# Performance work log

Hardware: AMD Instinct MI355X
Metric: run time of the kernel (lower is better)

Reference implementation:

```python
import jax, jax.numpy as jnp
import numpy as np

T, B, IN, H, L, C = 512, 4096, 12, 32, 10, 4


def setup_inputs() -> dict:
    key = jax.random.key(0)
    ks = jax.random.split(key, 12)
    s = 1.0 / np.sqrt(H)  # PyTorch GRU init scale ~ U(-1/sqrt(H), 1/sqrt(H))
    return {
        "x": jax.random.normal(ks[0], (T, B, IN), jnp.float32),
        "W_ih0": jax.random.normal(ks[1], (3 * H, IN), jnp.float32) * s,
        "W_hh0": jax.random.normal(ks[2], (3 * H, H), jnp.float32) * s,
        "b_ih0": jax.random.normal(ks[3], (3 * H,), jnp.float32) * s,
        "b_hh0": jax.random.normal(ks[4], (3 * H,), jnp.float32) * s,
        "W_ih": jax.random.normal(ks[5], (L - 1, 3 * H, H), jnp.float32) * s,
        "W_hh": jax.random.normal(ks[6], (L - 1, 3 * H, H), jnp.float32) * s,
        "b_ih": jax.random.normal(ks[7], (L - 1, 3 * H), jnp.float32) * s,
        "b_hh": jax.random.normal(ks[8], (L - 1, 3 * H), jnp.float32) * s,
        "fc_W": jax.random.normal(ks[9], (C, H), jnp.float32) * s,
        "fc_b": jax.random.normal(ks[10], (C,), jnp.float32) * s,
        "lengths": jax.random.randint(ks[11], (B,), 1, T + 1, jnp.int32),
    }


def gru_cell(x_t, h, Wi, Wh, bi, bh):
    # PyTorch GRU cell math
    gi = x_t @ Wi.T + bi          # [B, 3H]
    gh = h @ Wh.T + bh            # [B, 3H]
    i_r, i_z, i_n = jnp.split(gi, 3, axis=-1)
    h_r, h_z, h_n = jnp.split(gh, 3, axis=-1)
    r = jax.nn.sigmoid(i_r + h_r)
    z = jax.nn.sigmoid(i_z + h_z)
    n = jnp.tanh(i_n + r * h_n)
    return (1.0 - z) * n + z * h


def reference(x, W_ih0, W_hh0, b_ih0, b_hh0, W_ih, W_hh, b_ih, b_hh, fc_W, fc_b, lengths):
    Bn = x.shape[1]
    h0 = jnp.zeros((L, Bn, H), x.dtype)

    def step(h, x_t):
        hs = []
        inp = x_t
        for l in range(L):
            if l == 0:
                hl = gru_cell(inp, h[0], W_ih0, W_hh0, b_ih0, b_hh0)
            else:
                hl = gru_cell(inp, h[l], W_ih[l - 1], W_hh[l - 1], b_ih[l - 1], b_hh[l - 1])
            hs.append(hl)
            inp = hl
        return jnp.stack(hs), inp  # carry all-layer hidden, emit top-layer output

    _, outs = jax.lax.scan(step, h0, x)  # [T, B, H]
    idx = jnp.maximum(lengths, 1) - 1    # last valid timestep per sequence
    last = outs[idx, jnp.arange(Bn)]     # [B, H]
    logits = last @ fc_W.T + fc_b        # [B, C]
    return jax.nn.log_softmax(logits, axis=1)
```

## Files before the change

### kernel.cpp

```cpp
#include <hip/hip_runtime.h>
#include <math.h>

#define TT 512
#define BB 4096
#define IN_DIM 12
#define HH 32
#define LL 10
#define CC 4
#define NTH (LL * 64)
#define SS (TT / 2 + LL - 1)

typedef _Float16 half8 __attribute__((ext_vector_type(8)));
typedef _Float16 half4 __attribute__((ext_vector_type(4)));
typedef float f32x4 __attribute__((ext_vector_type(4)));

#define LOG2E 1.44269504088896340736f

#define H_HI 0
#define H_LO (LL * 4 * 512)
#define X_HI (H_LO + LL * 2 * 512)
#define LDS16_TOT (X_HI + 2 * 512)

#define MFMA_(A, B, C) C = __builtin_amdgcn_mfma_f32_16x16x32_f16(A, B, C, 0, 0, 0)

__global__ __launch_bounds__(NTH, 2)
void gru_fused_mfma(const float* __restrict__ x,
                    const float* __restrict__ Wih0,
                    const float* __restrict__ Whh0,
                    const float* __restrict__ bih0,
                    const float* __restrict__ bhh0,
                    const float* __restrict__ Wih,
                    const float* __restrict__ Whh,
                    const float* __restrict__ bih,
                    const float* __restrict__ bhh,
                    const int*   __restrict__ lengths,
                    float*       __restrict__ last)
{
    __shared__ __align__(16) _Float16 lds16[LDS16_TOT];

    const int tid  = threadIdx.x;
    const int w    = tid >> 6;
    const int lane = tid & 63;
    const int bi16 = lane & 15;
    const int quad = lane >> 4;
    const int bg   = blockIdx.x;

    {
        float4 z4 = make_float4(0.f, 0.f, 0.f, 0.f);
        float4* p = (float4*)lds16;
        for (int i = tid; i < LDS16_TOT / 8; i += NTH) p[i] = z4;
    }
    __syncthreads();

    const float *Wi, *Wh, *bivec, *bhvec;
    int wistride;
    if (w == 0) { Wi = Wih0; Wh = Whh0; bivec = bih0; bhvec = bhh0; wistride = IN_DIM; }
    else {
        Wi = Wih + (size_t)(w - 1) * 96 * HH;
        Wh = Whh + (size_t)(w - 1) * 96 * HH;
        bivec = bih + (size_t)(w - 1) * 96;
        bhvec = bhh + (size_t)(w - 1) * 96;
        wistride = HH;
    }

    const int frow[12] = {0, 0, 16, 16, 32, 32, 48, 48, 64, 80, 64, 80};
    const int fchk[12] = {0, 1, 0, 1, 0, 1, 0, 1, 0, 0, 1, 1};
    half8 Whi[12], Wlo[6];
#pragma unroll
    for (int f = 0; f < 12; f++) {
        const float sc = (f < 8) ? -LOG2E : 2.0f * LOG2E;
        int row = frow[f] + bi16;
        const float* src; int kin;
        if (fchk[f] == 0) { src = Wi + (size_t)row * wistride; kin = wistride; }
        else              { src = Wh + (size_t)row * HH;       kin = HH; }
        int wloidx = (f < 8) ? (f >> 1) : (f - 6);
#pragma unroll
        for (int kk = 0; kk < 8; kk++) {
            int k = quad * 8 + kk;
            float v = (k < kin) ? src[k] * sc : 0.0f;
            _Float16 h = (_Float16)v;
            Whi[f][kk] = h;
            if (fchk[f] == 1) Wlo[wloidx][kk] = (_Float16)(v - (float)h);
        }
    }

    f32x4 biasreg[8];
#pragma unroll
    for (int ct = 0; ct < 8; ct++) {
        int g = ct >> 1, jt = ct & 1;
#pragma unroll
        for (int r = 0; r < 4; r++) {
            int j = jt * 16 + quad * 4 + r;
            float v;
            if      (g == 0) v = -(bivec[j]      + bhvec[j])      * LOG2E;
            else if (g == 1) v = -(bivec[32 + j] + bhvec[32 + j]) * LOG2E;
            else if (g == 2) v = bivec[64 + j] * (2.0f * LOG2E);
            else             v = bhvec[64 + j] * (2.0f * LOG2E);
            biasreg[ct][r] = v;
        }
    }

    int capT = -1;
    if (w == LL - 1) {
        int len = lengths[bg * 16 + bi16];
        capT = ((len < 1) ? 1 : len) - 1;
    }

    const int laneoff = lane * 8;
    const int inbase  = (w == 0) ? X_HI : (H_HI + (w - 1) * 2048);
    const int inmask  = (w == 0) ? 1 : 3;
    const int ownhi   = H_HI + w * 2048;
    const int ownlo   = H_LO + w * 1024;
    const int wibase  = (quad >> 1) * 128 + bi16 * 8 + (quad & 1) * 4;

    const int xbb = lane / 3, xkg = lane - xbb * 3;
    const int xq   = (xkg == 2) ? 1 : 0;
    const int xoff = (xkg == 1) ? 4 : 0;
    const int xidx = xq * 128 + xbb * 8 + xoff;
    const bool xlane = (w == 0) && (lane < 48);

    auto stage_x = [&](const float4& xl, int t) {
        half4 h4;
        h4[0] = (_Float16)xl.x; h4[1] = (_Float16)xl.y;
        h4[2] = (_Float16)xl.z; h4[3] = (_Float16)xl.w;
        *(half4*)(lds16 + X_HI + ((t & 1) << 9) + xidx) = h4;
    };

    if (xlane) {
        float4 x0 = *(const float4*)(x + (size_t)bg * 192 + lane * 4);
        float4 x1 = *(const float4*)(x + (size_t)BB * IN_DIM + (size_t)bg * 192 + lane * 4);
        stage_x(x0, 0);
        stage_x(x1, 1);
    }

    float hprev[8] = {0, 0, 0, 0, 0, 0, 0, 0};
    __syncthreads();

    auto substep = [&](int t) {
        half8 bxh = *(const half8*)(lds16 + inbase + ((t & inmask) << 9) + laneoff);
        half8 bhh = *(const half8*)(lds16 + ownhi + (((t + 3) & 3) << 9) + laneoff);
        half8 bhl = *(const half8*)(lds16 + ownlo + (((t + 1) & 1) << 9) + laneoff);

        f32x4 acc[8];
#pragma unroll
        for (int ct = 0; ct < 8; ct++) acc[ct] = biasreg[ct];

#pragma unroll
        for (int ct = 0; ct < 4; ct++) {
            MFMA_(Whi[ct * 2 + 0], bxh, acc[ct]);
            MFMA_(Whi[ct * 2 + 1], bhh, acc[ct]);
            MFMA_(Whi[ct * 2 + 1], bhl, acc[ct]);
            MFMA_(Wlo[ct],         bhh, acc[ct]);
        }
#pragma unroll
        for (int jt = 0; jt < 2; jt++) {
            MFMA_(Whi[8 + jt],  bxh, acc[4 + jt]);
            MFMA_(Whi[10 + jt], bhh, acc[6 + jt]);
            MFMA_(Whi[10 + jt], bhl, acc[6 + jt]);
            MFMA_(Wlo[4 + jt],  bhh, acc[6 + jt]);
        }

#pragma unroll
        for (int jt = 0; jt < 2; jt++) {
            f32x4 R = acc[0 + jt], Z = acc[2 + jt];
            f32x4 IN_ = acc[4 + jt], HN = acc[6 + jt];
            half4 h4, l4;
            float hv[4];
#pragma unroll
            for (int r = 0; r < 4; r++) {
                float rv = __builtin_amdgcn_rcpf(1.0f + __builtin_amdgcn_exp2f(R[r]));
                float zv = __builtin_amdgcn_rcpf(1.0f + __builtin_amdgcn_exp2f(Z[r]));
                float ea = __builtin_amdgcn_exp2f(fmaf(rv, HN[r], IN_[r]));
                float nv = fmaf(-2.0f, __builtin_amdgcn_rcpf(ea + 1.0f), 1.0f);
                float h  = fmaf(zv, hprev[jt * 4 + r] - nv, nv);
                hprev[jt * 4 + r] = h;
                _Float16 hh16 = (_Float16)h;
                h4[r] = hh16;
                l4[r] = (_Float16)(h - (float)hh16);
                hv[r] = h;
            }
            int wi = jt * 256 + wibase;
            *(half4*)(lds16 + ownhi + ((t & 3) << 9) + wi) = h4;
            *(half4*)(lds16 + ownlo + ((t & 1) << 9) + wi) = l4;
            if (w == LL - 1 && t == capT) {
                float4 o = make_float4(hv[0], hv[1], hv[2], hv[3]);
                *(float4*)(last + (size_t)(bg * 16 + bi16) * HH + jt * 16 + quad * 4) = o;
            }
        }
    };

    for (int s = 0; s < SS; ++s) {
        const bool active = (unsigned)(s - w) < (unsigned)(TT / 2);
        const int t0 = 2 * (s - w);

        float4 xa0, xa1;
        bool dl0 = false, dl1 = false;
        if (xlane && active) {
            if (t0 + 2 < TT) {
                xa0 = *(const float4*)(x + (size_t)(t0 + 2) * BB * IN_DIM +
                                       (size_t)bg * 192 + lane * 4);
                dl0 = true;
            }
            if (t0 + 3 < TT) {
                xa1 = *(const float4*)(x + (size_t)(t0 + 3) * BB * IN_DIM +
                                       (size_t)bg * 192 + lane * 4);
                dl1 = true;
            }
        }

        if (active) {
            substep(t0);
            substep(t0 + 1);
        }
        if (dl0) stage_x(xa0, t0 + 2);
        if (dl1) stage_x(xa1, t0 + 3);

        __syncthreads();
    }
}

__global__ __launch_bounds__(256)
void fc_head(const float* __restrict__ last,
             const float* __restrict__ fcW,
             const float* __restrict__ fcb,
             float* __restrict__ out)
{
    int b = blockIdx.x * blockDim.x + threadIdx.x;
    if (b >= BB) return;
    float lg[CC];
#pragma unroll
    for (int c = 0; c < CC; c++) lg[c] = fcb[c];
#pragma unroll
    for (int j = 0; j < HH; j++) {
        float h = last[(size_t)b * HH + j];
#pragma unroll
        for (int c = 0; c < CC; c++) lg[c] = fmaf(fcW[c * HH + j], h, lg[c]);
    }
    float m = lg[0];
#pragma unroll
    for (int c = 1; c < CC; c++) m = fmaxf(m, lg[c]);
    float s = 0.0f;
#pragma unroll
    for (int c = 0; c < CC; c++) s += __expf(lg[c] - m);
    float lse = m + logf(s);
#pragma unroll
    for (int c = 0; c < CC; c++) out[(size_t)b * CC + c] = lg[c] - lse;
}

extern "C" void kernel_launch(void* const* d_in, const int* in_sizes, int n_in,
                              void* d_out, int out_size, void* d_ws, size_t ws_size,
                              hipStream_t stream)
{
    const float* x    = (const float*)d_in[0];
    const float* Wih0 = (const float*)d_in[1];
    const float* Whh0 = (const float*)d_in[2];
    const float* bih0 = (const float*)d_in[3];
    const float* bhh0 = (const float*)d_in[4];
    const float* Wih  = (const float*)d_in[5];
    const float* Whh  = (const float*)d_in[6];
    const float* bih  = (const float*)d_in[7];
    const float* bhh  = (const float*)d_in[8];
    const float* fcW  = (const float*)d_in[9];
    const float* fcb  = (const float*)d_in[10];
    const int*   lens = (const int*)d_in[11];
    float* out = (float*)d_out;

    float* last = (float*)d_ws;

    gru_fused_mfma<<<dim3(BB / 16), dim3(NTH), 0, stream>>>(
        x, Wih0, Whh0, bih0, bhh0, Wih, Whh, bih, bhh, lens, last);

    fc_head<<<dim3(BB / 256), dim3(256), 0, stream>>>(last, fcW, fcb, out);
}
```

Before: 980.3 us.

## Replace block-wide barriers with per-wave LDS flag handshakes in layer wavefront

Replaces the global per-step __syncthreads in the layer-pipelined wavefront with point-to-point producer/consumer flags in LDS. Each layer wave waits on its upstream neighbour's forward flag and its downstream neighbour's consumption flag, so waves can drift apart instead of moving in lockstep. This removes the barrier cost and the idle waiting at pipeline fill and drain. In exchange it relies on spin-waits with s_sleep and on the ring-buffer depth being enough for the allowed slack. Memory ordering across waves rests on atomic acquire/release at workgroup scope.

```diff
diff --git a/kernel.cpp b/kernel.cpp
--- a/kernel.cpp
+++ b/kernel.cpp
@@ -8,7 +8,6 @@
 #define LL 10
 #define CC 4
 #define NTH (LL * 64)
-#define SS (TT / 2 + LL - 1)
 
 typedef _Float16 half8 __attribute__((ext_vector_type(8)));
 typedef _Float16 half4 __attribute__((ext_vector_type(4)));
@@ -37,6 +36,8 @@
                     float*       __restrict__ last)
 {
     __shared__ __align__(16) _Float16 lds16[LDS16_TOT];
+    __shared__ int flagS[LL];
+    __shared__ int rflagS[LL];
 
     const int tid  = threadIdx.x;
     const int w    = tid >> 6;
@@ -50,6 +51,7 @@
         float4* p = (float4*)lds16;
         for (int i = tid; i < LDS16_TOT / 8; i += NTH) p[i] = z4;
     }
+    if (lane == 0) { flagS[w] = -1; rflagS[w] = -1; }
     __syncthreads();
 
     const float *Wi, *Wh, *bivec, *bhvec;
@@ -189,33 +191,47 @@
         }
     };
 
-    for (int s = 0; s < SS; ++s) {
-        const bool active = (unsigned)(s - w) < (unsigned)(TT / 2);
-        const int t0 = 2 * (s - w);
+    for (int t = 0; t < TT; t += 2) {
+        if (w > 0) {
+            while (__hip_atomic_load(&flagS[w - 1], __ATOMIC_ACQUIRE,
+                                     __HIP_MEMORY_SCOPE_WORKGROUP) < t + 1)
+                __builtin_amdgcn_s_sleep(1);
+        }
+        if (w < LL - 1) {
+            while (__hip_atomic_load(&rflagS[w], __ATOMIC_ACQUIRE,
+                                     __HIP_MEMORY_SCOPE_WORKGROUP) < t - 3)
+                __builtin_amdgcn_s_sleep(1);
+        }
 
         float4 xa0, xa1;
         bool dl0 = false, dl1 = false;
-        if (xlane && active) {
-            if (t0 + 2 < TT) {
-                xa0 = *(const float4*)(x + (size_t)(t0 + 2) * BB * IN_DIM +
+        if (xlane) {
+            if (t + 2 < TT) {
+                xa0 = *(const float4*)(x + (size_t)(t + 2) * BB * IN_DIM +
                                        (size_t)bg * 192 + lane * 4);
                 dl0 = true;
             }
-            if (t0 + 3 < TT) {
-                xa1 = *(const float4*)(x + (size_t)(t0 + 3) * BB * IN_DIM +
+            if (t + 3 < TT) {
+                xa1 = *(const float4*)(x + (size_t)(t + 3) * BB * IN_DIM +
                                        (size_t)bg * 192 + lane * 4);
                 dl1 = true;
             }
         }
 
-        if (active) {
-            substep(t0);
-            substep(t0 + 1);
-        }
-        if (dl0) stage_x(xa0, t0 + 2);
-        if (dl1) stage_x(xa1, t0 + 3);
-
-        __syncthreads();
+        substep(t);
+        substep(t + 1);
+
+        if (dl0) stage_x(xa0, t + 2);
+        if (dl1) stage_x(xa1, t + 3);
+
+        if (lane == 0) {
+            if (w < LL - 1)
+                __hip_atomic_store(&flagS[w], t + 1, __ATOMIC_RELEASE,
+                                   __HIP_MEMORY_SCOPE_WORKGROUP);
+            if (w > 0)
+                __hip_atomic_store(&rflagS[w - 1], t + 1, __ATOMIC_RELEASE,
+                                   __HIP_MEMORY_SCOPE_WORKGROUP);
+        }
     }
 }
 
```

After: 958.6 us. 1.02x faster.
